# Kernel tuning notes

Measured on AMD Instinct MI355X. Metric: run time of the kernel, lower is better.

The kernel has to match this reference:

```python
import jax, jax.numpy as jnp
import numpy as np

TAU = 0.5
EPS = 1e-8


def _mlp(x, W1, b1, W2, b2):
    # torch nn.Linear: y = x @ W.T + b
    h = jax.nn.elu(x @ W1.T + b1)
    return h @ W2.T + b2


def setup_inputs() -> dict:
    key = jax.random.key(0)
    ks = jax.random.split(key, 10)
    N, D = 8192, 256
    gain = 1.414
    std = gain * np.sqrt(2.0 / (D + D))  # xavier_normal_
    inp = {
        "z1": jax.random.normal(ks[0], (N, D), dtype=jnp.float32),
        "z2": jax.random.normal(ks[1], (N, D), dtype=jnp.float32),
        "W1c": std * jax.random.normal(ks[2], (D, D), dtype=jnp.float32),
        "b1c": jnp.zeros((D,), dtype=jnp.float32),
        "W2c": std * jax.random.normal(ks[3], (D, D), dtype=jnp.float32),
        "b2c": jnp.zeros((D,), dtype=jnp.float32),
        "W1k": std * jax.random.normal(ks[4], (D, D), dtype=jnp.float32),
        "b1k": jnp.zeros((D,), dtype=jnp.float32),
        "W2k": std * jax.random.normal(ks[5], (D, D), dtype=jnp.float32),
        "b2k": jnp.zeros((D,), dtype=jnp.float32),
        "cl_size": N,
    }
    return inp


def reference(z1, z2, W1c, b1c, W2c, b2c, W1k, b1k, W2k, b2k, cl_size):
    z1p = _mlp(z1, W1c, b1c, W2c, b2c)  # [N, D]
    z2p = _mlp(z2, W1k, b1k, W2k, b2k)  # [N, D]
    n1 = jnp.linalg.norm(z1p, axis=-1, keepdims=True)  # [N, 1]
    n2 = jnp.linalg.norm(z2p, axis=-1, keepdims=True)  # [N, 1]
    dot = z1p @ z2p.T                                  # [N, N]
    sim = jnp.exp(dot / (n1 * n2.T) / TAU)
    sim = sim / (jnp.sum(sim, axis=1, keepdims=True) + EPS)
    pos = jnp.diagonal(sim)                            # diag(sim * I).sum(-1)
    return -jnp.mean(jnp.log(pos))
```

## Files before the change

### kernel.cpp

```cpp
#include <hip/hip_runtime.h>
#include <hip/hip_fp8.h>

typedef __bf16 bf16;
typedef __bf16 bf16x8 __attribute__((ext_vector_type(8)));
typedef __bf16 bf16x4v __attribute__((ext_vector_type(4)));
typedef float  f32x4  __attribute__((ext_vector_type(4)));

#define NROWS 8192
#define DDIM  256
#define TAU_INV 2.0f
#define KAPPA 2.8853900817779268f
#define LN2 0.6931471805599453f
#define EPS 1e-8f

#define AS1C(p) ((const __attribute__((address_space(1))) void*)(p))
#define AS3(p)  ((__attribute__((address_space(3))) void*)(p))

static __device__ __forceinline__ bf16x8 cvt8(f32x4 a, f32x4 b) {
  bf16x8 o;
  o[0] = (bf16)a[0]; o[1] = (bf16)a[1]; o[2] = (bf16)a[2]; o[3] = (bf16)a[3];
  o[4] = (bf16)b[0]; o[5] = (bf16)b[1]; o[6] = (bf16)b[2]; o[7] = (bf16)b[3];
  return o;
}

static __device__ __forceinline__ unsigned char f2fp8(float x) {
  __hip_fp8_e4m3 q(x);
  return (unsigned char)q.__x;
}

__global__ __launch_bounds__(256) void cast4_kernel(
    const float* __restrict__ s0, const float* __restrict__ s1,
    const float* __restrict__ s2, const float* __restrict__ s3,
    bf16* __restrict__ dst) {
  const float* s = blockIdx.y == 0 ? s0 : blockIdx.y == 1 ? s1 : blockIdx.y == 2 ? s2 : s3;
  bf16* d = dst + (size_t)blockIdx.y * 65536;
  int i = blockIdx.x * 256 + threadIdx.x;
  f32x4 v = ((const f32x4*)s)[i];
  bf16x4v o;
  o[0] = (bf16)v[0]; o[1] = (bf16)v[1]; o[2] = (bf16)v[2]; o[3] = (bf16)v[3];
  ((bf16x4v*)d)[i] = o;
}

__global__ __launch_bounds__(512, 1) void mlp_norm_kernel(
    const float* __restrict__ z1f, const float* __restrict__ z2f,
    const bf16* __restrict__ wq,
    const float* __restrict__ b1c, const float* __restrict__ b2c,
    const float* __restrict__ b1k, const float* __restrict__ b2k,
    unsigned char* __restrict__ outA, unsigned char* __restrict__ outB)
{
  const int view = blockIdx.y;
  const float* xf = view ? z2f : z1f;
  const bf16*  w1 = wq + (size_t)view * 131072;
  const bf16*  w2 = w1 + 65536;
  const float* b1 = view ? b1k : b1c;
  const float* b2 = view ? b2k : b2c;
  unsigned char* out = view ? outB : outA;
  const float osc = view ? 1.0f : KAPPA;

  __shared__ __align__(16) char xs[64 * 512];
  __shared__ __align__(16) char hs[64 * 512];
  __shared__ float sspart[8][64];

  const int tid  = threadIdx.x;
  const int lane = tid & 63;
  const int w    = tid >> 6;
  const int c    = lane & 15;
  const int g    = lane >> 4;
  const int r0   = blockIdx.x * 64;
  const int colw = w * 32;

#pragma unroll
  for (int k = 0; k < 4; ++k) {
    int gid = k * 512 + tid;
    int row = gid >> 5, cg = gid & 31;
    const f32x4* p = (const f32x4*)(xf + (size_t)(r0 + row) * DDIM + cg * 8);
    *(bf16x8*)(xs + row * 512 + ((cg * 16) ^ ((row & 7) << 4))) = cvt8(p[0], p[1]);
  }
  __syncthreads();

  float b1v[2], b2v[2];
#pragma unroll
  for (int ct = 0; ct < 2; ++ct) {
    b1v[ct] = b1[colw + ct * 16 + c];
    b2v[ct] = b2[colw + ct * 16 + c];
  }

  const int aswz = (c & 7) << 4;
  const bf16* w1base = w1 + (size_t)(colw + c) * DDIM + g * 8;
  const bf16* w2base = w2 + (size_t)(colw + c) * DDIM + g * 8;

  f32x4 acc[2][4];
  const f32x4 fz = {0.f, 0.f, 0.f, 0.f};
#pragma unroll
  for (int ct = 0; ct < 2; ++ct)
#pragma unroll
    for (int mt = 0; mt < 4; ++mt) acc[ct][mt] = fz;

  bf16x8 wcur[2], wnxt[2];
#pragma unroll
  for (int ct = 0; ct < 2; ++ct)
    wcur[ct] = *(const bf16x8*)(w1base + (size_t)ct * 16 * DDIM);
#pragma unroll
  for (int ks = 0; ks < 8; ++ks) {
    if (ks < 7) {
#pragma unroll
      for (int ct = 0; ct < 2; ++ct)
        wnxt[ct] = *(const bf16x8*)(w1base + (size_t)ct * 16 * DDIM + (ks + 1) * 32);
    }
    bf16x8 af[4];
#pragma unroll
    for (int mt = 0; mt < 4; ++mt)
      af[mt] = *(const bf16x8*)(xs + (mt * 16 + c) * 512 + ((ks * 64 + g * 16) ^ aswz));
#pragma unroll
    for (int ct = 0; ct < 2; ++ct)
#pragma unroll
      for (int mt = 0; mt < 4; ++mt)
        acc[ct][mt] = __builtin_amdgcn_mfma_f32_16x16x32_bf16(af[mt], wcur[ct], acc[ct][mt], 0, 0, 0);
#pragma unroll
    for (int ct = 0; ct < 2; ++ct) wcur[ct] = wnxt[ct];
  }

#pragma unroll
  for (int ct = 0; ct < 2; ++ct)
#pragma unroll
    for (int mt = 0; mt < 4; ++mt)
#pragma unroll
      for (int r = 0; r < 4; ++r) {
        float pre = acc[ct][mt][r] + b1v[ct];
        float h = pre > 0.0f ? pre : (__expf(pre) - 1.0f);
        int row = mt * 16 + g * 4 + r;
        int cb = (colw + ct * 16 + c) * 2;
        *(bf16*)(hs + row * 512 + (cb ^ ((row & 7) << 4))) = (bf16)h;
      }
  __syncthreads();

#pragma unroll
  for (int ct = 0; ct < 2; ++ct)
#pragma unroll
    for (int mt = 0; mt < 4; ++mt) acc[ct][mt] = fz;

#pragma unroll
  for (int ct = 0; ct < 2; ++ct)
    wcur[ct] = *(const bf16x8*)(w2base + (size_t)ct * 16 * DDIM);
#pragma unroll
  for (int ks = 0; ks < 8; ++ks) {
    if (ks < 7) {
#pragma unroll
      for (int ct = 0; ct < 2; ++ct)
        wnxt[ct] = *(const bf16x8*)(w2base + (size_t)ct * 16 * DDIM + (ks + 1) * 32);
    }
    bf16x8 af[4];
#pragma unroll
    for (int mt = 0; mt < 4; ++mt)
      af[mt] = *(const bf16x8*)(hs + (mt * 16 + c) * 512 + ((ks * 64 + g * 16) ^ aswz));
#pragma unroll
    for (int ct = 0; ct < 2; ++ct)
#pragma unroll
      for (int mt = 0; mt < 4; ++mt)
        acc[ct][mt] = __builtin_amdgcn_mfma_f32_16x16x32_bf16(af[mt], wcur[ct], acc[ct][mt], 0, 0, 0);
#pragma unroll
    for (int ct = 0; ct < 2; ++ct) wcur[ct] = wnxt[ct];
  }

  float ss[4][4];
#pragma unroll
  for (int mt = 0; mt < 4; ++mt)
#pragma unroll
    for (int r = 0; r < 4; ++r) ss[mt][r] = 0.f;
#pragma unroll
  for (int ct = 0; ct < 2; ++ct)
#pragma unroll
    for (int mt = 0; mt < 4; ++mt)
#pragma unroll
      for (int r = 0; r < 4; ++r) {
        float z = acc[ct][mt][r] + b2v[ct];
        acc[ct][mt][r] = z;
        ss[mt][r] += z * z;
      }
#pragma unroll
  for (int m = 1; m < 16; m <<= 1)
#pragma unroll
    for (int mt = 0; mt < 4; ++mt)
#pragma unroll
      for (int r = 0; r < 4; ++r) ss[mt][r] += __shfl_xor(ss[mt][r], m, 64);

  if (c == 0) {
#pragma unroll
    for (int mt = 0; mt < 4; ++mt)
#pragma unroll
      for (int r = 0; r < 4; ++r) sspart[w][mt * 16 + g * 4 + r] = ss[mt][r];
  }
  __syncthreads();

#pragma unroll
  for (int mt = 0; mt < 4; ++mt)
#pragma unroll
    for (int r = 0; r < 4; ++r) {
      int row = mt * 16 + g * 4 + r;
      float s = (sspart[0][row] + sspart[1][row]) + (sspart[2][row] + sspart[3][row])
              + (sspart[4][row] + sspart[5][row]) + (sspart[6][row] + sspart[7][row]);
      float rinv = osc / sqrtf(s);
      int hswp = ((row >> 2) & 1) << 3;
#pragma unroll
      for (int ct = 0; ct < 2; ++ct)
        out[(size_t)(r0 + row) * DDIM + ((colw + ct * 16 + c) ^ hswp)]
            = f2fp8(acc[ct][mt][r] * rinv);
    }
}

__global__ __launch_bounds__(256, 2) void lse_kernel(
    const unsigned char* __restrict__ A, const unsigned char* __restrict__ B,
    float* __restrict__ partial, float* __restrict__ diagdot)
{
  __shared__ __align__(16) char As[128 * 64];
  __shared__ __align__(16) char Bs[128 * 64];

  const int tid  = threadIdx.x;
  const int lane = tid & 63;
  const int w    = tid >> 6;
  const int c    = lane & 15;
  const int g    = lane >> 4;
  const int brow = blockIdx.y * 128;
  const int bcol = blockIdx.x * 128;
  const int wrow = (w >> 1) * 64;
  const int wcol = (w & 1) * 64;

  f32x4 acc[4][4];
  const f32x4 fz = {0.f, 0.f, 0.f, 0.f};
#pragma unroll
  for (int i = 0; i < 4; ++i)
#pragma unroll
    for (int j = 0; j < 4; ++j) acc[i][j] = fz;

  for (int kt = 0; kt < 4; ++kt) {
#pragma unroll
    for (int it = 0; it < 2; ++it) {
      int slot = it * 256 + tid;
      int row = slot >> 2, q = slot & 3;
      int col = kt * 64 + ((q ^ (row & 3)) << 4);
      __builtin_amdgcn_global_load_lds(AS1C(A + (size_t)(brow + row) * DDIM + col),
                                       AS3(As + slot * 16), 16, 0, 0);
      __builtin_amdgcn_global_load_lds(AS1C(B + (size_t)(bcol + row) * DDIM + col),
                                       AS3(Bs + slot * 16), 16, 0, 0);
    }
    __syncthreads();
#pragma unroll
    for (int sk = 0; sk < 2; ++sk) {
      long af[4], bfv[4];
#pragma unroll
      for (int mt = 0; mt < 4; ++mt) {
        int rl = wrow + mt * 16 + c;
        af[mt] = *(const long*)(As + rl * 64
                  + ((((sk << 1) | (g >> 1)) ^ (rl & 3)) << 4)
                  + (((g & 1) ^ ((rl >> 2) & 1)) << 3));
      }
#pragma unroll
      for (int ct = 0; ct < 4; ++ct) {
        int rl = wcol + ct * 16 + c;
        bfv[ct] = *(const long*)(Bs + rl * 64
                  + ((((sk << 1) | (g >> 1)) ^ (rl & 3)) << 4)
                  + (((g & 1) ^ ((rl >> 2) & 1)) << 3));
      }
#pragma unroll
      for (int mt = 0; mt < 4; ++mt)
#pragma unroll
        for (int ct = 0; ct < 4; ++ct)
          acc[mt][ct] = __builtin_amdgcn_mfma_f32_16x16x32_fp8_fp8(af[mt], bfv[ct], acc[mt][ct], 0, 0, 0);
    }
    __syncthreads();
  }

  if (blockIdx.x == blockIdx.y && (w == 0 || w == 3) && (c >> 2) == g) {
#pragma unroll
    for (int mt = 0; mt < 4; ++mt) {
      f32x4 a = acc[mt][mt];
      int r = c & 3;
      float dv = (r == 0) ? a[0] : (r == 1) ? a[1] : (r == 2) ? a[2] : a[3];
      diagdot[brow + wrow + mt * 16 + c] = dv;
    }
  }

  float rs[4][4];
#pragma unroll
  for (int mt = 0; mt < 4; ++mt)
#pragma unroll
    for (int r = 0; r < 4; ++r) rs[mt][r] = 0.f;
#pragma unroll
  for (int mt = 0; mt < 4; ++mt)
#pragma unroll
    for (int ct = 0; ct < 4; ++ct)
#pragma unroll
      for (int r = 0; r < 4; ++r) rs[mt][r] += __builtin_amdgcn_exp2f(acc[mt][ct][r]);
#pragma unroll
  for (int m = 1; m < 16; m <<= 1)
#pragma unroll
    for (int mt = 0; mt < 4; ++mt)
#pragma unroll
      for (int r = 0; r < 4; ++r) rs[mt][r] += __shfl_xor(rs[mt][r], m, 64);

  if (c == 0) {
    int cb2 = blockIdx.x * 2 + (w & 1);
#pragma unroll
    for (int mt = 0; mt < 4; ++mt)
#pragma unroll
      for (int r = 0; r < 4; ++r) {
        int grow = brow + wrow + mt * 16 + g * 4 + r;
        partial[(size_t)grow * 128 + cb2] = rs[mt][r];
      }
  }
}

__global__ __launch_bounds__(256) void rowfinal_kernel(
    const float* __restrict__ partial, const float* __restrict__ diagdot,
    float* __restrict__ blocksum)
{
  int gid = blockIdx.x * 256 + threadIdx.x;
  int row = gid >> 2, q = gid & 3;
  const f32x4* p = (const f32x4*)(partial + (size_t)row * 128 + q * 32);
  float s = 0.f;
#pragma unroll
  for (int i = 0; i < 8; ++i) {
    f32x4 v = p[i];
    s += (v[0] + v[1]) + (v[2] + v[3]);
  }
  s += __shfl_xor(s, 1, 64);
  s += __shfl_xor(s, 2, 64);
  float term = (q == 0) ? (logf(s + EPS) - diagdot[row] * LN2) : 0.f;
#pragma unroll
  for (int m = 1; m < 64; m <<= 1) term += __shfl_xor(term, m, 64);
  __shared__ float part[4];
  if ((threadIdx.x & 63) == 0) part[threadIdx.x >> 6] = term;
  __syncthreads();
  if (threadIdx.x == 0) blocksum[blockIdx.x] = part[0] + part[1] + part[2] + part[3];
}

__global__ __launch_bounds__(128) void final_kernel(const float* __restrict__ blocksum,
                                                    float* __restrict__ out)
{
  int tid = threadIdx.x;
  float s = blocksum[tid];
#pragma unroll
  for (int m = 1; m < 64; m <<= 1) s += __shfl_xor(s, m, 64);
  __shared__ float p[2];
  if ((tid & 63) == 0) p[tid >> 6] = s;
  __syncthreads();
  if (tid == 0) out[0] = (p[0] + p[1]) * (1.0f / NROWS);
}

extern "C" void kernel_launch(void* const* d_in, const int* in_sizes, int n_in,
                              void* d_out, int out_size, void* d_ws, size_t ws_size,
                              hipStream_t stream) {
  const float* z1  = (const float*)d_in[0];
  const float* z2  = (const float*)d_in[1];
  const float* W1c = (const float*)d_in[2];
  const float* b1c = (const float*)d_in[3];
  const float* W2c = (const float*)d_in[4];
  const float* b2c = (const float*)d_in[5];
  const float* W1k = (const float*)d_in[6];
  const float* b1k = (const float*)d_in[7];
  const float* W2k = (const float*)d_in[8];
  const float* b2k = (const float*)d_in[9];

  char* ws = (char*)d_ws;
  unsigned char* aU = (unsigned char*)(ws);
  unsigned char* bU = (unsigned char*)(ws + (size_t)2 * 1024 * 1024);
  float* partial  = (float*)(ws + (size_t)4  * 1024 * 1024);
  float* diagdot  = (float*)(ws + (size_t)8  * 1024 * 1024);
  float* blocksum = (float*)(ws + (size_t)8  * 1024 * 1024 + 64 * 1024);
  bf16*  wq       = (bf16*)(ws + (size_t)9  * 1024 * 1024);

  cast4_kernel<<<dim3(64, 4), 256, 0, stream>>>(W1c, W2c, W1k, W2k, wq);

  mlp_norm_kernel<<<dim3(NROWS / 64, 2), 512, 0, stream>>>(
      z1, z2, wq, b1c, b2c, b1k, b2k, aU, bU);

  lse_kernel<<<dim3(NROWS / 128, NROWS / 128), 256, 0, stream>>>(aU, bU, partial, diagdot);

  rowfinal_kernel<<<128, 256, 0, stream>>>(partial, diagdot, blocksum);
  final_kernel<<<1, 128, 0, stream>>>(blocksum, (float*)d_out);
}
```

Baseline: 69.31 us.

## Double-buffer LDS tiles in lse_kernel to overlap global loads with MFMA

Replaces the single As/Bs LDS tiles with a two-stage ping-pong buffer. The next K-tile is prefetched with global_load_lds while the current one is consumed, using explicit vmcnt waits and raw barriers in place of __syncthreads, and the K loop is fully unrolled. The aim is to hide global-to-LDS latency behind the MFMA work. LDS use per block doubles to 32KB, which may affect occupancy at 2 blocks per CU, and the hand-written waitcnt values must match the number of outstanding loads.

After: 68.15 us, median of 2. About the same (-1.7%).

```diff
diff --git a/kernel.cpp b/kernel.cpp
--- a/kernel.cpp
+++ b/kernel.cpp
@@ -212,8 +212,7 @@
     const unsigned char* __restrict__ A, const unsigned char* __restrict__ B,
     float* __restrict__ partial, float* __restrict__ diagdot)
 {
-  __shared__ __align__(16) char As[128 * 64];
-  __shared__ __align__(16) char Bs[128 * 64];
+  __shared__ __align__(16) char lds[32768];
 
   const int tid  = threadIdx.x;
   const int lane = tid & 63;
@@ -225,6 +224,21 @@
   const int wrow = (w >> 1) * 64;
   const int wcol = (w & 1) * 64;
 
+#define STAGE(ttt)                                                                   \
+  {                                                                                  \
+    const int bsel_ = ((ttt) & 1) * 16384;                                           \
+    _Pragma("unroll")                                                                \
+    for (int it = 0; it < 2; ++it) {                                                 \
+      int slot = it * 256 + tid;                                                     \
+      int row = slot >> 2, q = slot & 3;                                             \
+      int col = (ttt) * 64 + ((q ^ (row & 3)) << 4);                                 \
+      __builtin_amdgcn_global_load_lds(AS1C(A + (size_t)(brow + row) * DDIM + col),  \
+                                       AS3(lds + bsel_ + slot * 16), 16, 0, 0);      \
+      __builtin_amdgcn_global_load_lds(AS1C(B + (size_t)(bcol + row) * DDIM + col),  \
+                                       AS3(lds + bsel_ + 8192 + slot * 16), 16, 0, 0); \
+    }                                                                                \
+  }
+
   f32x4 acc[4][4];
   const f32x4 fz = {0.f, 0.f, 0.f, 0.f};
 #pragma unroll
@@ -232,18 +246,23 @@
 #pragma unroll
     for (int j = 0; j < 4; ++j) acc[i][j] = fz;
 
+  STAGE(0);
+
+#pragma unroll
   for (int kt = 0; kt < 4; ++kt) {
-#pragma unroll
-    for (int it = 0; it < 2; ++it) {
-      int slot = it * 256 + tid;
-      int row = slot >> 2, q = slot & 3;
-      int col = kt * 64 + ((q ^ (row & 3)) << 4);
-      __builtin_amdgcn_global_load_lds(AS1C(A + (size_t)(brow + row) * DDIM + col),
-                                       AS3(As + slot * 16), 16, 0, 0);
-      __builtin_amdgcn_global_load_lds(AS1C(B + (size_t)(bcol + row) * DDIM + col),
-                                       AS3(Bs + slot * 16), 16, 0, 0);
-    }
-    __syncthreads();
+    __builtin_amdgcn_s_barrier();
+    asm volatile("" ::: "memory");
+    if (kt < 3) {
+      STAGE(kt + 1);
+      asm volatile("s_waitcnt vmcnt(4)" ::: "memory");
+    } else {
+      asm volatile("s_waitcnt vmcnt(0)" ::: "memory");
+    }
+    __builtin_amdgcn_s_barrier();
+    asm volatile("" ::: "memory");
+
+    const char* As = lds + (kt & 1) * 16384;
+    const char* Bs = As + 8192;
 #pragma unroll
     for (int sk = 0; sk < 2; ++sk) {
       long af[4], bfv[4];
@@ -267,8 +286,8 @@
         for (int ct = 0; ct < 4; ++ct)
           acc[mt][ct] = __builtin_amdgcn_mfma_f32_16x16x32_fp8_fp8(af[mt], bfv[ct], acc[mt][ct], 0, 0, 0);
     }
-    __syncthreads();
-  }
+  }
+#undef STAGE
 
   if (blockIdx.x == blockIdx.y && (w == 0 || w == 3) && (c >> 2) == g) {
 #pragma unroll
```
